# Kernel optimization log

Hardware: AMD Instinct MI355X
Metric: run time of the kernel (lower is better)

The kernel has to match this reference:

```python
import jax, jax.numpy as jnp
import numpy as np

IN_FEATURES = 4096
OUT_FEATURES = 4096


def fht(x):
    """Normalized fast Walsh-Hadamard transform along last axis (n = power of 2).
    Equals x @ H_n / sqrt(n); matches matmul_hadU(t)_cuda when had_K is None (K=1)."""
    n = x.shape[-1]
    orig_shape = x.shape
    x = x.reshape(-1, n)
    h = 1
    while h < n:
        x = x.reshape(-1, n // (2 * h), 2, h)
        a = x[:, :, 0, :]
        b = x[:, :, 1, :]
        x = jnp.stack([a + b, a - b], axis=2).reshape(-1, n)
        h *= 2
    scale = jnp.asarray(1.0 / np.sqrt(n), dtype=x.dtype)
    return (x * scale).reshape(orig_shape)


def decode_e8p(Qidxs, grid_abs):
    """E8P12-style decode: each 16-bit codeword -> 8 fp16 weights.
    Low 8 bits index a 256-entry table of 8 absolute values; high 8 bits are
    per-element sign flips. Returns dense W of shape [out, in]."""
    idx = Qidxs.astype(jnp.int32) & 0xFFFF            # [out, in/8]
    abs_vals = grid_abs[idx & 0xFF]                   # [out, in/8, 8]
    sbits = (idx[..., None] >> (8 + jnp.arange(8, dtype=jnp.int32))) & 1
    signs = (1 - 2 * sbits).astype(grid_abs.dtype)    # [out, in/8, 8] in {+1,-1}
    w = abs_vals * signs
    return w.reshape(Qidxs.shape[0], -1)              # [out, in]


def setup_inputs() -> dict:
    key = jax.random.key(0)
    k1, k2, k3, k4, k5, k6 = jax.random.split(key, 6)
    inp = {}
    inp["input"] = jax.random.normal(k1, (2, 4096, IN_FEATURES), dtype=jnp.float16)
    inp["Qidxs"] = jax.random.randint(k2, (OUT_FEATURES, IN_FEATURES // 8), 0, 65536, dtype=jnp.int32)
    # abs half-integer-ish grid values (E8 lattice magnitudes live in ~[0.25, 3.75])
    inp["grid_abs"] = (jax.random.uniform(k3, (256, 8), dtype=jnp.float32) * 3.0 + 0.25).astype(jnp.float16)
    # SU/SV are random sign vectors in QuIP
    inp["SU"] = (1 - 2 * jax.random.bernoulli(k4, 0.5, (IN_FEATURES,)).astype(jnp.float16))
    inp["SV"] = (1 - 2 * jax.random.bernoulli(k5, 0.5, (OUT_FEATURES,)).astype(jnp.float16))
    inp["Wscale"] = jnp.ones((), dtype=jnp.float32)
    inp["bias"] = jax.random.normal(k6, (OUT_FEATURES,), dtype=jnp.float16) * jnp.float16(0.01)
    return inp


def reference(input, Qidxs, grid_abs, SU, SV, Wscale, bias):
    x = input.reshape(-1, input.shape[-1])            # [T, in]
    x = x * SU                                        # input sign rescale
    x = fht(x)                                        # H^T x / sqrt(n) (H symmetric)
    x = (x * Wscale).astype(jnp.float16)              # global weight scale
    W = decode_e8p(Qidxs, grid_abs)                   # [out, in] dequantized lattice weights
    out = jnp.dot(x, W.T, preferred_element_type=jnp.float32).astype(jnp.float16)  # [T, out]
    out = fht(out)                                    # output Hadamard
    out = out * SV + bias                             # output sign rescale + bias
    return out.reshape(*input.shape[:-1], out.shape[-1])
```

## Files before the change

### kernel.cpp

```cpp
#include <hip/hip_runtime.h>
#include <hip/hip_bf16.h>
#include <stdint.h>

typedef _Float16 f16;
typedef _Float16 f16x8 __attribute__((ext_vector_type(8)));
typedef float f32x4 __attribute__((ext_vector_type(4)));

#define N_FEAT 4096
#define M_ROWS 8192
#define QSTRIDE 512

#define GLD16(gptr, lptr)                                                      \
  __builtin_amdgcn_global_load_lds(                                            \
      (const __attribute__((address_space(1))) void*)(gptr),                   \
      (__attribute__((address_space(3))) void*)(uint32_t)(uintptr_t)(lptr),    \
      16, 0, 0)

#define PAD64(i) ((i) + (((i) >> 6) << 2))

__device__ __forceinline__ void fht16(float v[16]) {
#pragma unroll
  for (int h = 1; h < 16; h <<= 1) {
#pragma unroll
    for (int i = 0; i < 16; i += (h << 1)) {
#pragma unroll
      for (int j = 0; j < h; ++j) {
        float a = v[i + j], b = v[i + j + h];
        v[i + j] = a + b;
        v[i + j + h] = a - b;
      }
    }
  }
}

__device__ __forceinline__ void fht4(float& a, float& b, float& c, float& d) {
  float t0 = a + b, t1 = a - b, t2 = c + d, t3 = c - d;
  a = t0 + t2; b = t1 + t3; c = t0 - t2; d = t1 - t3;
}

__global__ __launch_bounds__(256) void k_fht_in(const float* __restrict__ x,
                                                const float* __restrict__ SU,
                                                const float* __restrict__ wscale,
                                                f16* __restrict__ out) {
  __shared__ float lds[4096 + 256];
  const int row = blockIdx.x;
  const int t = threadIdx.x;
  const float* xr = x + (size_t)row * N_FEAT;
  float v[16];

#pragma unroll
  for (int j = 0; j < 4; ++j) {
    const float4 a = *(const float4*)(xr + (t << 4) + 4 * j);
    const float4 s = *(const float4*)(SU + (t << 4) + 4 * j);
    v[4 * j + 0] = a.x * s.x; v[4 * j + 1] = a.y * s.y;
    v[4 * j + 2] = a.z * s.z; v[4 * j + 3] = a.w * s.w;
  }
  fht16(v);
#pragma unroll
  for (int j = 0; j < 4; ++j)
    *(float4*)&lds[PAD64((t << 4) + 4 * j)] =
        make_float4(v[4 * j], v[4 * j + 1], v[4 * j + 2], v[4 * j + 3]);
  __syncthreads();

  const int a = t & 15, b = t >> 4;
#pragma unroll
  for (int j = 0; j < 16; ++j) v[j] = lds[PAD64((b << 8) + (j << 4) + a)];
  fht16(v);
#pragma unroll
  for (int j = 0; j < 16; ++j) lds[PAD64((b << 8) + (j << 4) + a)] = v[j];
  __syncthreads();

#pragma unroll
  for (int j = 0; j < 16; ++j) v[j] = lds[PAD64((j << 8) + t)];
  fht16(v);
  const float s = wscale[0] * 0.015625f;
  f16* op = out + (size_t)row * N_FEAT;
#pragma unroll
  for (int j = 0; j < 16; ++j) op[(j << 8) + t] = (f16)(v[j] * s);
}

__global__ __launch_bounds__(256) void k_wA(const int* __restrict__ q,
                                            const float* __restrict__ grid,
                                            f16* __restrict__ Wp) {
  __shared__ float tabf[2048];
  __shared__ float tile[64 * 65];
  const int t = threadIdx.x;
  const int kg = blockIdx.x;
  const int ng = blockIdx.y;
  {
    *(float4*)&tabf[t * 8] = *(const float4*)(grid + t * 8);
    *(float4*)&tabf[t * 8 + 4] = *(const float4*)(grid + t * 8 + 4);
  }
  __syncthreads();

#pragma unroll
  for (int e2 = 0; e2 < 2; ++e2) {
    const int e = t + (e2 << 8);
    const int nl = e >> 3, c = e & 7;
    const unsigned code =
        (unsigned)q[(size_t)(ng * 64 + nl) * QSTRIDE + kg * 8 + c] & 0xffffu;
    const float* tb = &tabf[(code & 255u) * 8];
#pragma unroll
    for (int j = 0; j < 8; ++j) {
      const int bi = __float_as_int(tb[j]) ^ (int)(((code >> (8 + j)) & 1u) << 31);
      tile[nl * 65 + (c << 3) + j] = __int_as_float(bi);
    }
  }
  __syncthreads();

  {
    const int k = t & 63, p = t >> 6;
    float v[16];
#pragma unroll
    for (int j = 0; j < 16; ++j) v[j] = tile[(16 * p + j) * 65 + k];
    fht16(v);
#pragma unroll
    for (int j = 0; j < 16; ++j) tile[(16 * p + j) * 65 + k] = v[j];
  }
  __syncthreads();

  {
    const int k = t & 63, base = (t >> 6) << 2;
#pragma unroll
    for (int bb = 0; bb < 4; ++bb) {
      const int low = base + bb;
      float v0 = tile[(low) * 65 + k],      v1 = tile[(low + 16) * 65 + k];
      float v2 = tile[(low + 32) * 65 + k], v3 = tile[(low + 48) * 65 + k];
      fht4(v0, v1, v2, v3);
      tile[(low) * 65 + k] = v0;      tile[(low + 16) * 65 + k] = v1;
      tile[(low + 32) * 65 + k] = v2; tile[(low + 48) * 65 + k] = v3;
    }
  }
  __syncthreads();

  {
    const int nl = t >> 2, koff = (t & 3) << 4;
    union { f16 h[16]; int4 v[2]; } u;
#pragma unroll
    for (int i = 0; i < 16; ++i) u.h[i] = (f16)tile[nl * 65 + koff + i];
    int4* dst = (int4*)(Wp + (size_t)(ng * 64 + nl) * N_FEAT + kg * 64 + koff);
    dst[0] = u.v[0];
    dst[1] = u.v[1];
  }
}

__global__ __launch_bounds__(256) void k_wB(f16* __restrict__ Wp) {
  __shared__ float tile[64 * 65];
  const int t = threadIdx.x;
  const int kg = blockIdx.x;
  const int n0 = blockIdx.y;
  {
    const int n1 = t >> 2, koff = (t & 3) << 4;
    const f16* src = Wp + (size_t)(n0 + 64 * n1) * N_FEAT + kg * 64 + koff;
    union { f16 h[16]; int4 v[2]; } u;
    u.v[0] = ((const int4*)src)[0];
    u.v[1] = ((const int4*)src)[1];
#pragma unroll
    for (int i = 0; i < 16; ++i) tile[n1 * 65 + koff + i] = (float)u.h[i];
  }
  __syncthreads();
  {
    const int k = t & 63, p = t >> 6;
    float v[16];
#pragma unroll
    for (int j = 0; j < 16; ++j) v[j] = tile[(16 * p + j) * 65 + k];
    fht16(v);
#pragma unroll
    for (int j = 0; j < 16; ++j) tile[(16 * p + j) * 65 + k] = v[j];
  }
  __syncthreads();
  {
    const int k = t & 63, base = (t >> 6) << 2;
#pragma unroll
    for (int bb = 0; bb < 4; ++bb) {
      const int low = base + bb;
      float v0 = tile[(low) * 65 + k],      v1 = tile[(low + 16) * 65 + k];
      float v2 = tile[(low + 32) * 65 + k], v3 = tile[(low + 48) * 65 + k];
      fht4(v0, v1, v2, v3);
      tile[(low) * 65 + k] = v0;      tile[(low + 16) * 65 + k] = v1;
      tile[(low + 32) * 65 + k] = v2; tile[(low + 48) * 65 + k] = v3;
    }
  }
  __syncthreads();
  {
    const int n1 = t >> 2, koff = (t & 3) << 4;
    union { f16 h[16]; int4 v[2]; } u;
#pragma unroll
    for (int i = 0; i < 16; ++i) u.h[i] = (f16)tile[n1 * 65 + koff + i];
    int4* dst = (int4*)(Wp + (size_t)(n0 + 64 * n1) * N_FEAT + kg * 64 + koff);
    dst[0] = u.v[0];
    dst[1] = u.v[1];
  }
}

#define BM 128
#define BN 128
#define BK 64
#define KDIM 4096

__global__ __launch_bounds__(256) void k_gemm(const f16* __restrict__ A,
                                              const f16* __restrict__ B,
                                              float* __restrict__ C,
                                              const float* __restrict__ SV,
                                              const float* __restrict__ bias) {
  __shared__ __attribute__((aligned(16))) f16 sA[BM * BK];
  __shared__ __attribute__((aligned(16))) f16 sB[BN * BK];
  const int tid = threadIdx.x;
  const int lane = tid & 63;
  const int w = tid >> 6;
  const int wr = w >> 1, wc = w & 1;
  const int m0 = blockIdx.y * BM;
  const int n0 = blockIdx.x * BN;

  f32x4 acc[4][4];
#pragma unroll
  for (int i = 0; i < 4; ++i)
#pragma unroll
    for (int j = 0; j < 4; ++j) acc[i][j] = (f32x4)0.0f;

  const int srow = lane >> 3;
  const int scc = lane & 7;
  const int quad = lane >> 4;
  const int ml = lane & 15;

  for (int k0 = 0; k0 < KDIM; k0 += BK) {
#pragma unroll
    for (int i = 0; i < 4; ++i) {
      const int rb = ((w << 2) + i) << 3;
      const int r = rb + srow;
      const int kc = scc ^ (r & 7);
      GLD16(A + (size_t)(m0 + r) * KDIM + k0 + (kc << 3), &sA[rb << 6]);
    }
#pragma unroll
    for (int i = 0; i < 4; ++i) {
      const int rb = ((w << 2) + i) << 3;
      const int r = rb + srow;
      const int kc = scc ^ (r & 7);
      GLD16(B + (size_t)(n0 + r) * KDIM + k0 + (kc << 3), &sB[rb << 6]);
    }
    __syncthreads();

#pragma unroll
    for (int s = 0; s < 2; ++s) {
      f16x8 af[4], bfr[4];
#pragma unroll
      for (int i = 0; i < 4; ++i) {
        const int m = (wr << 6) + (i << 4) + ml;
        const int kc = ((s << 2) + quad) ^ (m & 7);
        af[i] = *(const f16x8*)&sA[(m << 6) + (kc << 3)];
      }
#pragma unroll
      for (int j = 0; j < 4; ++j) {
        const int n = (wc << 6) + (j << 4) + ml;
        const int kc = ((s << 2) + quad) ^ (n & 7);
        bfr[j] = *(const f16x8*)&sB[(n << 6) + (kc << 3)];
      }
#pragma unroll
      for (int i = 0; i < 4; ++i)
#pragma unroll
        for (int j = 0; j < 4; ++j)
          acc[i][j] = __builtin_amdgcn_mfma_f32_16x16x32_f16(af[i], bfr[j],
                                                             acc[i][j], 0, 0, 0);
    }
    __syncthreads();
  }

#pragma unroll
  for (int j = 0; j < 4; ++j) {
    const int col = n0 + (wc << 6) + (j << 4) + ml;
    const float sv = SV[col] * 0.015625f;
    const float bs = bias[col];
#pragma unroll
    for (int i = 0; i < 4; ++i) {
      const int rowb = m0 + (wr << 6) + (i << 4) + (quad << 2);
#pragma unroll
      for (int r = 0; r < 4; ++r)
        C[(size_t)(rowb + r) * N_FEAT + col] = acc[i][j][r] * sv + bs;
    }
  }
}

extern "C" void kernel_launch(void* const* d_in, const int* in_sizes, int n_in,
                              void* d_out, int out_size, void* d_ws, size_t ws_size,
                              hipStream_t stream) {
  const float* input = nullptr;
  const int* qidxs = nullptr;
  const float* grid_abs = nullptr;
  const float* wscale = nullptr;
  const float* v4k[3] = {nullptr, nullptr, nullptr};
  int n4 = 0;
  for (int i = 0; i < n_in; ++i) {
    switch (in_sizes[i]) {
      case 33554432: input = (const float*)d_in[i]; break;
      case 2097152:  qidxs = (const int*)d_in[i]; break;
      case 2048:     grid_abs = (const float*)d_in[i]; break;
      case 1:        wscale = (const float*)d_in[i]; break;
      case 4096:     if (n4 < 3) v4k[n4++] = (const float*)d_in[i]; break;
      default: break;
    }
  }
  const float* SU = v4k[0];
  const float* SV = v4k[1];
  const float* bias = v4k[2];

  f16* x = (f16*)d_ws;
  f16* Wp = (f16*)const_cast<float*>(input);
  float* out = (float*)d_out;

  k_fht_in<<<M_ROWS, 256, 0, stream>>>(input, SU, wscale, x);
  dim3 gw(64, 64);
  k_wA<<<gw, 256, 0, stream>>>(qidxs, grid_abs, Wp);
  k_wB<<<gw, 256, 0, stream>>>(Wp);
  dim3 g(N_FEAT / BN, M_ROWS / BM);
  k_gemm<<<g, 256, 0, stream>>>(x, Wp, out, SV, bias);
}
```

Baseline: 564.7 us.

## Rewrite GEMM as 256x256 double-buffered pipeline with interleaved loads and MFMA

The GEMM moves from 128x128 tiles with 4 waves to 256x256 tiles with 8 waves. It double-buffers LDS and splits each K-step into four quadrant phases, so the global-to-LDS loads for the next tile overlap the MFMAs on the current one. Explicit vmcnt waits, raw barriers, sched_barrier fences and setprio control the ordering. This aims to raise arithmetic intensity and hide load latency, at the cost of 128KB of LDS per block, more registers, and fragile hand-placed synchronization.

```diff
diff --git a/kernel.cpp b/kernel.cpp
--- a/kernel.cpp
+++ b/kernel.cpp
@@ -193,89 +193,158 @@
   }
 }
 
-#define BM 128
-#define BN 128
+#define BM 256
+#define BN 256
 #define BK 64
 #define KDIM 4096
 
-__global__ __launch_bounds__(256) void k_gemm(const f16* __restrict__ A,
-                                              const f16* __restrict__ B,
-                                              float* __restrict__ C,
-                                              const float* __restrict__ SV,
-                                              const float* __restrict__ bias) {
-  __shared__ __attribute__((aligned(16))) f16 sA[BM * BK];
-  __shared__ __attribute__((aligned(16))) f16 sB[BN * BK];
+#define WAITB(n)                                          \
+  asm volatile("s_waitcnt vmcnt(" #n ")" ::: "memory");   \
+  __builtin_amdgcn_s_barrier();
+
+#define SCHED_FENCE() __builtin_amdgcn_sched_barrier(0)
+
+#define STAGE_HALF(gbase, lhalf)                                         \
+  {                                                                      \
+    _Pragma("unroll")                                                    \
+    for (int i_ = 0; i_ < 2; ++i_) {                                     \
+      const int rb_ = (w << 4) + (i_ << 3);                              \
+      const int r_ = rb_ + srow;                                         \
+      const int kc_ = scc ^ (r_ & 7);                                    \
+      GLD16((gbase) + (size_t)r_ * KDIM + (kc_ << 3), (lhalf) + (rb_ << 6)); \
+    }                                                                    \
+  }
+
+#define LDA(dst, mh)                                                     \
+  {                                                                      \
+    _Pragma("unroll")                                                    \
+    for (int i_ = 0; i_ < 4; ++i_) {                                     \
+      const int m_ = ((mh) << 7) + (wr << 6) + (i_ << 4) + ml;           \
+      _Pragma("unroll")                                                  \
+      for (int s_ = 0; s_ < 2; ++s_) {                                   \
+        const int kc_ = ((s_ << 2) + quad) ^ (m_ & 7);                   \
+        dst[i_][s_] = *(const f16x8*)&sA[cur][(m_ << 6) + (kc_ << 3)];   \
+      }                                                                  \
+    }                                                                    \
+  }
+
+#define LDB(dst, nh)                                                     \
+  {                                                                      \
+    _Pragma("unroll")                                                    \
+    for (int j_ = 0; j_ < 2; ++j_) {                                     \
+      const int n_ = ((nh) << 7) + (wc << 5) + (j_ << 4) + ml;           \
+      _Pragma("unroll")                                                  \
+      for (int s_ = 0; s_ < 2; ++s_) {                                   \
+        const int kc_ = ((s_ << 2) + quad) ^ (n_ & 7);                   \
+        dst[j_][s_] = *(const f16x8*)&sB[cur][(n_ << 6) + (kc_ << 3)];   \
+      }                                                                  \
+    }                                                                    \
+  }
+
+#define MMAQ(mh, nh)                                                     \
+  {                                                                      \
+    __builtin_amdgcn_s_setprio(1);                                       \
+    _Pragma("unroll")                                                    \
+    for (int i_ = 0; i_ < 4; ++i_) {                                     \
+      _Pragma("unroll")                                                  \
+      for (int j_ = 0; j_ < 2; ++j_) {                                   \
+        acc[(mh) * 4 + i_][(nh) * 2 + j_] =                              \
+            __builtin_amdgcn_mfma_f32_16x16x32_f16(                      \
+                af[i_][0], bf[j_][0], acc[(mh) * 4 + i_][(nh) * 2 + j_], \
+                0, 0, 0);                                                \
+        acc[(mh) * 4 + i_][(nh) * 2 + j_] =                              \
+            __builtin_amdgcn_mfma_f32_16x16x32_f16(                      \
+                af[i_][1], bf[j_][1], acc[(mh) * 4 + i_][(nh) * 2 + j_], \
+                0, 0, 0);                                                \
+      }                                                                  \
+    }                                                                    \
+    __builtin_amdgcn_s_setprio(0);                                       \
+  }
+
+__global__ __launch_bounds__(512, 2) void k_gemm(const f16* __restrict__ A,
+                                                 const f16* __restrict__ B,
+                                                 float* __restrict__ C,
+                                                 const float* __restrict__ SV,
+                                                 const float* __restrict__ bias) {
+  __shared__ __attribute__((aligned(16))) f16 sA[2][BM * BK];
+  __shared__ __attribute__((aligned(16))) f16 sB[2][BN * BK];
+
   const int tid = threadIdx.x;
   const int lane = tid & 63;
   const int w = tid >> 6;
-  const int wr = w >> 1, wc = w & 1;
+  const int wr = w >> 2;
+  const int wc = w & 3;
   const int m0 = blockIdx.y * BM;
   const int n0 = blockIdx.x * BN;
-
-  f32x4 acc[4][4];
-#pragma unroll
-  for (int i = 0; i < 4; ++i)
-#pragma unroll
-    for (int j = 0; j < 4; ++j) acc[i][j] = (f32x4)0.0f;
-
+  const int quad = lane >> 4;
+  const int ml = lane & 15;
   const int srow = lane >> 3;
   const int scc = lane & 7;
-  const int quad = lane >> 4;
-  const int ml = lane & 15;
-
-  for (int k0 = 0; k0 < KDIM; k0 += BK) {
-#pragma unroll
-    for (int i = 0; i < 4; ++i) {
-      const int rb = ((w << 2) + i) << 3;
-      const int r = rb + srow;
-      const int kc = scc ^ (r & 7);
-      GLD16(A + (size_t)(m0 + r) * KDIM + k0 + (kc << 3), &sA[rb << 6]);
-    }
-#pragma unroll
-    for (int i = 0; i < 4; ++i) {
-      const int rb = ((w << 2) + i) << 3;
-      const int r = rb + srow;
-      const int kc = scc ^ (r & 7);
-      GLD16(B + (size_t)(n0 + r) * KDIM + k0 + (kc << 3), &sB[rb << 6]);
-    }
-    __syncthreads();
-
-#pragma unroll
-    for (int s = 0; s < 2; ++s) {
-      f16x8 af[4], bfr[4];
-#pragma unroll
-      for (int i = 0; i < 4; ++i) {
-        const int m = (wr << 6) + (i << 4) + ml;
-        const int kc = ((s << 2) + quad) ^ (m & 7);
-        af[i] = *(const f16x8*)&sA[(m << 6) + (kc << 3)];
-      }
-#pragma unroll
-      for (int j = 0; j < 4; ++j) {
-        const int n = (wc << 6) + (j << 4) + ml;
-        const int kc = ((s << 2) + quad) ^ (n & 7);
-        bfr[j] = *(const f16x8*)&sB[(n << 6) + (kc << 3)];
-      }
-#pragma unroll
-      for (int i = 0; i < 4; ++i)
-#pragma unroll
-        for (int j = 0; j < 4; ++j)
-          acc[i][j] = __builtin_amdgcn_mfma_f32_16x16x32_f16(af[i], bfr[j],
-                                                             acc[i][j], 0, 0, 0);
-    }
-    __syncthreads();
-  }
-
-#pragma unroll
-  for (int j = 0; j < 4; ++j) {
-    const int col = n0 + (wc << 6) + (j << 4) + ml;
+
+  f32x4 acc[8][4];
+#pragma unroll
+  for (int i = 0; i < 8; ++i)
+#pragma unroll
+    for (int j = 0; j < 4; ++j) acc[i][j] = (f32x4)0.0f;
+
+  const f16* Ab = A + (size_t)m0 * KDIM;
+  const f16* Bb = B + (size_t)n0 * KDIM;
+
+  STAGE_HALF(Ab, &sA[0][0]);
+  SCHED_FENCE();
+  STAGE_HALF(Bb, &sB[0][0]);
+  SCHED_FENCE();
+  STAGE_HALF(Bb + (size_t)128 * KDIM, &sB[0][128 * 64]);
+  SCHED_FENCE();
+  STAGE_HALF(Ab + (size_t)128 * KDIM, &sA[0][128 * 64]);
+  WAITB(4);
+
+  f16x8 af[4][2], bf[2][2];
+
+#pragma unroll 2
+  for (int t = 0; t < 64; ++t) {
+    const int cur = t & 1;
+    const int nxt = cur ^ 1;
+    const int kn = ((t + 1) & 63) << 6;
+    const f16* An = Ab + kn;
+    const f16* Bn = Bb + kn;
+
+    STAGE_HALF(An, &sA[nxt][0]);
+    LDA(af, 0);
+    LDB(bf, 0);
+    MMAQ(0, 0);
+
+    WAITB(4);
+    STAGE_HALF(Bn, &sB[nxt][0]);
+    LDB(bf, 1);
+    MMAQ(0, 1);
+
+    WAITB(4);
+    STAGE_HALF(Bn + (size_t)128 * KDIM, &sB[nxt][128 * 64]);
+    LDA(af, 1);
+    MMAQ(1, 1);
+
+    SCHED_FENCE();
+    STAGE_HALF(An + (size_t)128 * KDIM, &sA[nxt][128 * 64]);
+    LDB(bf, 0);
+    MMAQ(1, 0);
+    WAITB(4);
+  }
+
+  asm volatile("s_waitcnt vmcnt(0)" ::: "memory");
+
+#pragma unroll
+  for (int nj = 0; nj < 4; ++nj) {
+    const int col = n0 + ((nj >> 1) << 7) + (wc << 5) + ((nj & 1) << 4) + ml;
     const float sv = SV[col] * 0.015625f;
     const float bs = bias[col];
 #pragma unroll
-    for (int i = 0; i < 4; ++i) {
-      const int rowb = m0 + (wr << 6) + (i << 4) + (quad << 2);
+    for (int mi = 0; mi < 8; ++mi) {
+      const int rowb =
+          m0 + ((mi >> 2) << 7) + (wr << 6) + ((mi & 3) << 4) + (quad << 2);
 #pragma unroll
       for (int r = 0; r < 4; ++r)
-        C[(size_t)(rowb + r) * N_FEAT + col] = acc[i][j][r] * sv + bs;
+        C[(size_t)(rowb + r) * N_FEAT + col] = acc[mi][nj][r] * sv + bs;
     }
   }
 }
@@ -312,5 +381,5 @@
   k_wA<<<gw, 256, 0, stream>>>(qidxs, grid_abs, Wp);
   k_wB<<<gw, 256, 0, stream>>>(Wp);
   dim3 g(N_FEAT / BN, M_ROWS / BM);
-  k_gemm<<<g, 256, 0, stream>>>(x, Wp, out, SV, bias);
-}
+  k_gemm<<<g, 512, 0, stream>>>(x, Wp, out, SV, bias);
+}
```

Result: faster. 490.1 us (-13.2%).
